# Kernel tuning notes

Hardware: AMD Instinct MI355X
Metric: run time of the kernel (lower is better)

Reference implementation:

```python
import jax, jax.numpy as jnp
import numpy as np

B, NQ, NC, D, H = 4, 4096, 4096, 1024, 16
HD = D // H
LN_EPS = 1e-5


def _layernorm(x, g, b):
    mu = jnp.mean(x, axis=-1, keepdims=True)
    var = jnp.var(x, axis=-1, keepdims=True)
    return (x - mu) * jax.lax.rsqrt(var + LN_EPS) * g + b


def _kernel(x):
    # elu(x) + 1  (strictly positive feature map)
    return jax.nn.elu(x) + 1.0


def setup_inputs() -> dict:
    key = jax.random.key(0)
    ks = jax.random.split(key, 12)
    s = 1.0 / np.sqrt(D)
    return {
        "query": jax.random.normal(ks[0], (B, NQ, D), jnp.float32),
        "context": jax.random.normal(ks[1], (B, NC, D), jnp.float32),
        "q_w": jax.random.uniform(ks[2], (D, D), jnp.float32, -s, s),
        "q_b": jnp.zeros((D,), jnp.float32),
        "k_w": jax.random.uniform(ks[3], (D, D), jnp.float32, -s, s),
        "k_b": jnp.zeros((D,), jnp.float32),
        "v_w": jax.random.uniform(ks[4], (D, D), jnp.float32, -s, s),
        "v_b": jnp.zeros((D,), jnp.float32),
        "o_w": jax.random.uniform(ks[5], (D, D), jnp.float32, -s, s),
        "o_b": jnp.zeros((D,), jnp.float32),
        "lnq_g": jnp.ones((D,), jnp.float32),
        "lnq_b": jnp.zeros((D,), jnp.float32),
        "lnkv_g": jnp.ones((D,), jnp.float32),
        "lnkv_b": jnp.zeros((D,), jnp.float32),
    }


def reference(query, context, q_w, q_b, k_w, k_b, v_w, v_b, o_w, o_b,
              lnq_g, lnq_b, lnkv_g, lnkv_b):
    residual = query
    q = _layernorm(query, lnq_g, lnq_b)
    c = _layernorm(context, lnkv_g, lnkv_b)

    # torch Linear: y = x @ W.T + b ; reshape to (B, H, N, Hd)
    Q = (q @ q_w.T + q_b).reshape(B, NQ, H, HD).transpose(0, 2, 1, 3)
    K = (c @ k_w.T + k_b).reshape(B, NC, H, HD).transpose(0, 2, 1, 3)
    V = (c @ v_w.T + v_b).reshape(B, NC, H, HD).transpose(0, 2, 1, 3)

    Q = _kernel(Q)
    K = _kernel(K)

    # KV: (B, H, Hd, Hd) outer-product accumulation over context length
    KV = jnp.einsum("bhnd,bhne->bhde", K, V)
    K_sum = K.sum(axis=2)                              # (B, H, Hd)
    Z = jnp.einsum("bhqd,bhd->bhq", Q, K_sum)          # (B, H, Nq)
    Z = jnp.maximum(Z, 1e-6)

    out = jnp.einsum("bhqd,bhde->bhqe", Q, KV) / Z[..., None]
    out = out.transpose(0, 2, 1, 3).reshape(B, NQ, D)
    return residual + (out @ o_w.T + o_b)
```

## Files before the change

kernel.cpp:

```cpp
#include <hip/hip_runtime.h>

#define DEV __device__ __forceinline__

typedef __attribute__((ext_vector_type(8))) short short8;
typedef __attribute__((ext_vector_type(4))) short short4v;
typedef __attribute__((ext_vector_type(4))) float f32x4;

DEV float bf2f(unsigned short u) { return __uint_as_float(((unsigned int)u) << 16); }
DEV unsigned short f2bf(float f) {
    unsigned int u = __float_as_uint(f);
    u += 0x7FFFu + ((u >> 16) & 1u);
    return (unsigned short)(u >> 16);
}

DEV void gload_lds16(const void* g, void* l) {
    __builtin_amdgcn_global_load_lds(
        (__attribute__((address_space(1))) unsigned int*)(g),
        (__attribute__((address_space(3))) unsigned int*)(l),
        16, 0, 0);
}

#define NROW 16384
#define DDIM 1024

__global__ __launch_bounds__(256) void ln_kernel(
    const float* __restrict__ query, const float* __restrict__ context,
    const float* __restrict__ lnq_g, const float* __restrict__ lnq_b,
    const float* __restrict__ lnk_g, const float* __restrict__ lnk_b,
    unsigned short* __restrict__ qln, unsigned short* __restrict__ cln)
{
    const int row = blockIdx.x;
    const bool isq = row < NROW;
    const int r = isq ? row : row - NROW;
    const float* src = (isq ? query : context) + (size_t)r * DDIM;
    const float* g   = isq ? lnq_g : lnk_g;
    const float* bb  = isq ? lnq_b : lnk_b;
    unsigned short* dst = (isq ? qln : cln) + (size_t)r * DDIM;

    const int tid = threadIdx.x;
    f32x4 x = *(const f32x4*)(src + tid * 4);
    float s  = x[0] + x[1] + x[2] + x[3];
    float sq = x[0]*x[0] + x[1]*x[1] + x[2]*x[2] + x[3]*x[3];
#pragma unroll
    for (int off = 32; off; off >>= 1) {
        s  += __shfl_xor(s, off);
        sq += __shfl_xor(sq, off);
    }
    __shared__ float red[8];
    const int lane = tid & 63, w = tid >> 6;
    if (lane == 0) { red[w] = s; red[4 + w] = sq; }
    __syncthreads();
    s  = red[0] + red[1] + red[2] + red[3];
    sq = red[4] + red[5] + red[6] + red[7];
    const float mu  = s * (1.0f / DDIM);
    const float var = sq * (1.0f / DDIM) - mu * mu;
    const float rstd = rsqrtf(var + 1e-5f);

    f32x4 gv = *(const f32x4*)(g + tid * 4);
    f32x4 bv = *(const f32x4*)(bb + tid * 4);
    short4v o;
#pragma unroll
    for (int j = 0; j < 4; ++j)
        o[j] = (short)f2bf((x[j] - mu) * rstd * gv[j] + bv[j]);
    *(short4v*)(dst + tid * 4) = o;
}

__global__ __launch_bounds__(256) void conv_w(
    const float* __restrict__ a, const float* __restrict__ b,
    const float* __restrict__ c, const float* __restrict__ d,
    unsigned short* __restrict__ out)
{
    const int i = blockIdx.x * 256 + threadIdx.x;
    const int mat = i >> 18;
    const int idx = (i & 262143) * 4;
    const float* src = mat == 0 ? a : mat == 1 ? b : mat == 2 ? c : d;
    f32x4 v = *(const f32x4*)(src + idx);
    short4v o;
#pragma unroll
    for (int j = 0; j < 4; ++j) o[j] = (short)f2bf(v[j]);
    *(short4v*)(out + (size_t)mat * 1048576 + idx) = o;
}

template <int MODE>
__global__ __launch_bounds__(512, 2) void gemm_bt(
    const unsigned short* __restrict__ A, const unsigned short* __restrict__ Bm,
    void* __restrict__ Cout, const float* __restrict__ bias,
    const float* __restrict__ resid, int ldc)
{
    __shared__ __attribute__((aligned(16))) unsigned short smem[65536];
    unsigned short* sAb = smem;
    unsigned short* sBb = smem + 32768;

    const int bid = blockIdx.x;
    const int l = (bid & 7) * 32 + (bid >> 3);
    int m0, n0;
    if (MODE == 0 || MODE == 3) { m0 = (l >> 2) * 256; n0 = (l & 3) * 256; }
    else                        { m0 = (l & 3) * 256;  n0 = (l >> 2) * 256; }

    const int tid = threadIdx.x;
    const int lane = tid & 63, w = tid >> 6;
    const int wr = w >> 2, wc = w & 3;
    const int lr = lane & 15, lg = lane >> 4;

    const int srow = tid >> 3;
    const int cswz = (tid & 7) ^ (srow & 7);
    const unsigned short* gA0 = A  + (size_t)(m0 + srow) * 1024 + cswz * 8;
    const unsigned short* gB0 = Bm + (size_t)(n0 + srow) * 1024 + cswz * 8;

    const int sw0 = ((0 + lg) ^ (lr & 7)) * 8;
    const int sw1 = ((4 + lg) ^ (lr & 7)) * 8;

    f32x4 acc[8][4];
#pragma unroll
    for (int i = 0; i < 8; ++i)
#pragma unroll
        for (int j = 0; j < 4; ++j)
#pragma unroll
            for (int e = 0; e < 4; ++e) acc[i][j][e] = 0.0f;

#define STG(GP, SP, T)                                                        \
    {                                                                         \
        const unsigned short* g = (GP) + (T) * 64;                            \
        unsigned short* d = (SP) + ((T) & 1) * 16384 + tid * 8;               \
        _Pragma("unroll")                                                     \
        for (int L = 0; L < 4; ++L)                                           \
            gload_lds16(g + (size_t)L * 65536, d + L * 4096);                 \
    }

    STG(gB0, sBb, 0); STG(gA0, sAb, 0); STG(gB0, sBb, 1); STG(gA0, sAb, 1);

    for (int t = 0; t < 16; ++t) {
        const unsigned short* bA = sAb + (t & 1) * 16384;
        const unsigned short* bB = sBb + (t & 1) * 16384;
        short8 afl[4][2], afh[4][2], bvl[2][2], bvh[2][2];

        if (t == 15) asm volatile("s_waitcnt vmcnt(0)" ::: "memory");
        else         asm volatile("s_waitcnt vmcnt(8)" ::: "memory");
        __builtin_amdgcn_s_barrier();
#pragma unroll
        for (int mt = 0; mt < 4; ++mt) {
            const int ra = (wr * 128 + mt * 16 + lr) * 64;
            afl[mt][0] = *(const short8*)&bA[ra + sw0];
            afl[mt][1] = *(const short8*)&bA[ra + sw1];
        }
#pragma unroll
        for (int nt = 0; nt < 2; ++nt) {
            const int rb = (wc * 64 + nt * 16 + lr) * 64;
            bvl[nt][0] = *(const short8*)&bB[rb + sw0];
            bvl[nt][1] = *(const short8*)&bB[rb + sw1];
        }
        __builtin_amdgcn_s_setprio(1);
#pragma unroll
        for (int kk = 0; kk < 2; ++kk)
#pragma unroll
            for (int mt = 0; mt < 4; ++mt)
#pragma unroll
                for (int nt = 0; nt < 2; ++nt)
                    acc[mt][nt] = __builtin_amdgcn_mfma_f32_16x16x32_bf16(
                        afl[mt][kk], bvl[nt][kk], acc[mt][nt], 0, 0, 0);
        __builtin_amdgcn_s_setprio(0);
        asm volatile("s_waitcnt lgkmcnt(0)" ::: "memory");
        __builtin_amdgcn_s_barrier();

#pragma unroll
        for (int nt = 0; nt < 2; ++nt) {
            const int rb = (wc * 64 + (nt + 2) * 16 + lr) * 64;
            bvh[nt][0] = *(const short8*)&bB[rb + sw0];
            bvh[nt][1] = *(const short8*)&bB[rb + sw1];
        }
        __builtin_amdgcn_s_setprio(1);
#pragma unroll
        for (int kk = 0; kk < 2; ++kk)
#pragma unroll
            for (int mt = 0; mt < 4; ++mt)
#pragma unroll
                for (int nt = 0; nt < 2; ++nt)
                    acc[mt][nt + 2] = __builtin_amdgcn_mfma_f32_16x16x32_bf16(
                        afl[mt][kk], bvh[nt][kk], acc[mt][nt + 2], 0, 0, 0);
        __builtin_amdgcn_s_setprio(0);
        asm volatile("s_waitcnt lgkmcnt(0)" ::: "memory");
        __builtin_amdgcn_s_barrier();

#pragma unroll
        for (int mt = 0; mt < 4; ++mt) {
            const int ra = (wr * 128 + (mt + 4) * 16 + lr) * 64;
            afh[mt][0] = *(const short8*)&bA[ra + sw0];
            afh[mt][1] = *(const short8*)&bA[ra + sw1];
        }
        if (t + 2 < 16) STG(gB0, sBb, t + 2);
        __builtin_amdgcn_s_setprio(1);
#pragma unroll
        for (int kk = 0; kk < 2; ++kk)
#pragma unroll
            for (int mt = 0; mt < 4; ++mt)
#pragma unroll
                for (int nt = 0; nt < 2; ++nt)
                    acc[mt + 4][nt + 2] = __builtin_amdgcn_mfma_f32_16x16x32_bf16(
                        afh[mt][kk], bvh[nt][kk], acc[mt + 4][nt + 2], 0, 0, 0);
        __builtin_amdgcn_s_setprio(0);
        asm volatile("s_waitcnt lgkmcnt(0)" ::: "memory");
        __builtin_amdgcn_s_barrier();

        if (t + 2 < 16) STG(gA0, sAb, t + 2);
        __builtin_amdgcn_s_setprio(1);
#pragma unroll
        for (int kk = 0; kk < 2; ++kk)
#pragma unroll
            for (int mt = 0; mt < 4; ++mt)
#pragma unroll
                for (int nt = 0; nt < 2; ++nt)
                    acc[mt + 4][nt] = __builtin_amdgcn_mfma_f32_16x16x32_bf16(
                        afh[mt][kk], bvl[nt][kk], acc[mt + 4][nt], 0, 0, 0);
        __builtin_amdgcn_s_setprio(0);
    }
#undef STG

#pragma unroll
    for (int mt = 0; mt < 8; ++mt) {
#pragma unroll
        for (int nt = 0; nt < 4; ++nt) {
            const int col = n0 + wc * 64 + nt * 16 + lr;
#pragma unroll
            for (int i = 0; i < 4; ++i) {
                const int row = m0 + wr * 128 + mt * 16 + lg * 4 + i;
                float v = acc[mt][nt][i];
                if (MODE == 0) { v += bias[col]; v = v > 0.0f ? v + 1.0f : __expf(v); }
                if (MODE == 1) { v += bias[row]; v = v > 0.0f ? v + 1.0f : __expf(v); }
                if (MODE == 2) { v += bias[row]; }
                if (MODE == 3) { v += bias[col] + resid[(size_t)row * 1024 + col]; }
                if (MODE == 3)
                    ((float*)Cout)[(size_t)row * 1024 + col] = v;
                else
                    ((unsigned short*)Cout)[(size_t)row * (size_t)ldc + col] = f2bf(v);
            }
        }
    }
}

__global__ __launch_bounds__(256) void kv_kernel(
    const unsigned short* __restrict__ VT, const unsigned short* __restrict__ KT,
    float* __restrict__ KVTp)
{
    const int bh = blockIdx.x, sp = blockIdx.y;
    const int b = bh >> 4, h = bh & 15;
    const int tid = threadIdx.x, lane = tid & 63, w = tid >> 6;
    const int lr = lane & 15, lg = lane >> 4;

    f32x4 acc[4][4];
#pragma unroll
    for (int i = 0; i < 4; ++i)
#pragma unroll
        for (int j = 0; j < 4; ++j)
#pragma unroll
            for (int e = 0; e < 4; ++e) acc[i][j][e] = 0.0f;

    const size_t colbase = (size_t)b * 4096 + sp * 1024 + w * 256 + lg * 8;
    const unsigned short* va = VT + (size_t)(h * 64 + lr) * NROW + colbase;
    const unsigned short* ka = KT + (size_t)(h * 64 + lr) * NROW + colbase;

    for (int ks = 0; ks < 8; ++ks) {
        short8 af[4], bfv[4];
#pragma unroll
        for (int mt = 0; mt < 4; ++mt)
            af[mt] = *(const short8*)(va + (size_t)mt * 16 * NROW + ks * 32);
#pragma unroll
        for (int nt = 0; nt < 4; ++nt)
            bfv[nt] = *(const short8*)(ka + (size_t)nt * 16 * NROW + ks * 32);
#pragma unroll
        for (int mt = 0; mt < 4; ++mt)
#pragma unroll
            for (int nt = 0; nt < 4; ++nt)
                acc[mt][nt] = __builtin_amdgcn_mfma_f32_16x16x32_bf16(
                    af[mt], bfv[nt], acc[mt][nt], 0, 0, 0);
    }

    __shared__ float red4[4][4096];
#pragma unroll
    for (int mt = 0; mt < 4; ++mt)
#pragma unroll
        for (int nt = 0; nt < 4; ++nt)
#pragma unroll
            for (int i = 0; i < 4; ++i)
                red4[w][(mt * 16 + lg * 4 + i) * 64 + nt * 16 + lr] = acc[mt][nt][i];
    __syncthreads();
    float* out = KVTp + ((size_t)sp * 64 + bh) * 4096;
    for (int i = tid; i < 4096; i += 256)
        out[i] = red4[0][i] + red4[1][i] + red4[2][i] + red4[3][i];
}

__global__ __launch_bounds__(256) void ksum_kernel(
    const unsigned short* __restrict__ KT, float* __restrict__ Ksum)
{
    const int bh = blockIdx.x, quad = blockIdx.y;
    const int b = bh >> 4, h = bh & 15;
    const int tid = threadIdx.x, lane = tid & 63, w = tid >> 6;
    const int dbase = quad * 16 + w * 4;
#pragma unroll
    for (int dd = 0; dd < 4; ++dd) {
        const int d = dbase + dd;
        const unsigned short* p = KT + (size_t)(h * 64 + d) * NROW + b * 4096 + lane * 8;
        float s = 0.0f;
#pragma unroll
        for (int it = 0; it < 8; ++it) {
            short8 v = *(const short8*)(p + it * 512);
#pragma unroll
            for (int j = 0; j < 8; ++j) s += bf2f((unsigned short)v[j]);
        }
#pragma unroll
        for (int off = 32; off; off >>= 1) s += __shfl_xor(s, off);
        if (lane == 0) Ksum[bh * 64 + d] = s;
    }
}

__global__ __launch_bounds__(256) void z_kernel(
    const unsigned short* __restrict__ Q, const float* __restrict__ Ksum,
    float* __restrict__ invZ)
{
    const int gid = blockIdx.x * 256 + threadIdx.x;
    const int n = gid >> 4, h = gid & 15;
    const int b = n >> 12;
    const unsigned short* q = Q + (size_t)n * DDIM + h * 64;
    const float* ks = Ksum + ((b << 4) + h) * 64;
    float z = 0.0f;
#pragma unroll
    for (int it = 0; it < 8; ++it) {
        short8 v = *(const short8*)(q + it * 8);
#pragma unroll
        for (int j = 0; j < 8; ++j) z += bf2f((unsigned short)v[j]) * ks[it * 8 + j];
    }
    invZ[gid] = 1.0f / fmaxf(z, 1e-6f);
}

__global__ __launch_bounds__(256) void a2_kernel(
    const unsigned short* __restrict__ Q, const float* __restrict__ KVTp,
    const float* __restrict__ invZ, unsigned short* __restrict__ A2)
{
    const int m0 = blockIdx.x * 128, h = blockIdx.y;
    const int b = m0 >> 12, bh = (b << 4) + h;
    const int tid = threadIdx.x, lane = tid & 63, w = tid >> 6;
    const int wr = w >> 1, wc = w & 1;
    const int lr = lane & 15, lg = lane >> 4;

    f32x4 acc[4][2];
#pragma unroll
    for (int i = 0; i < 4; ++i)
#pragma unroll
        for (int j = 0; j < 2; ++j)
#pragma unroll
            for (int e = 0; e < 4; ++e) acc[i][j][e] = 0.0f;

    const unsigned short* qa = Q + (size_t)(m0 + wr * 64 + lr) * DDIM + h * 64 + lg * 8;
    const float* kvb = KVTp + (size_t)bh * 4096 + (wc * 32 + lr) * 64 + lg * 8;

#pragma unroll
    for (int ks = 0; ks < 2; ++ks) {
        short8 af[4];
#pragma unroll
        for (int mt = 0; mt < 4; ++mt)
            af[mt] = *(const short8*)(qa + (size_t)mt * 16 * DDIM + ks * 32);
        short8 bfv[2];
#pragma unroll
        for (int nt = 0; nt < 2; ++nt) {
            const float* p = kvb + nt * 16 * 64 + ks * 32;
            short8 t;
#pragma unroll
            for (int j = 0; j < 8; ++j) {
                float v = p[j] + p[j + 262144] + p[j + 2 * 262144] + p[j + 3 * 262144];
                t[j] = (short)f2bf(v);
            }
            bfv[nt] = t;
        }
#pragma unroll
        for (int mt = 0; mt < 4; ++mt)
#pragma unroll
            for (int nt = 0; nt < 2; ++nt)
                acc[mt][nt] = __builtin_amdgcn_mfma_f32_16x16x32_bf16(
                    af[mt], bfv[nt], acc[mt][nt], 0, 0, 0);
    }

#pragma unroll
    for (int mt = 0; mt < 4; ++mt)
#pragma unroll
        for (int nt = 0; nt < 2; ++nt)
#pragma unroll
            for (int i = 0; i < 4; ++i) {
                const int row = m0 + wr * 64 + mt * 16 + lg * 4 + i;
                const int col = h * 64 + wc * 32 + nt * 16 + lr;
                const float v = acc[mt][nt][i] * invZ[row * 16 + h];
                A2[(size_t)row * DDIM + col] = f2bf(v);
            }
}

extern "C" void kernel_launch(void* const* d_in, const int* in_sizes, int n_in,
                              void* d_out, int out_size, void* d_ws, size_t ws_size,
                              hipStream_t stream)
{
    const float* query   = (const float*)d_in[0];
    const float* context = (const float*)d_in[1];
    const float* q_w = (const float*)d_in[2];
    const float* q_b = (const float*)d_in[3];
    const float* k_w = (const float*)d_in[4];
    const float* k_b = (const float*)d_in[5];
    const float* v_w = (const float*)d_in[6];
    const float* v_b = (const float*)d_in[7];
    const float* o_w = (const float*)d_in[8];
    const float* o_b = (const float*)d_in[9];
    const float* lnq_g = (const float*)d_in[10];
    const float* lnq_b = (const float*)d_in[11];
    const float* lnk_g = (const float*)d_in[12];
    const float* lnk_b = (const float*)d_in[13];

    char* ws = (char*)d_ws;
    unsigned short* WQ  = (unsigned short*)(ws);
    unsigned short* WK  = (unsigned short*)(ws + (2u << 20));
    unsigned short* WV  = (unsigned short*)(ws + (4u << 20));
    unsigned short* WO  = (unsigned short*)(ws + (6u << 20));
    unsigned short* QLN = (unsigned short*)(ws + (8u << 20));
    unsigned short* CLN = (unsigned short*)(ws + (40u << 20));
    unsigned short* Qm  = (unsigned short*)(ws + (72u << 20));
    unsigned short* KT  = (unsigned short*)(ws + (104u << 20));
    unsigned short* VT  = (unsigned short*)(ws + (136u << 20));
    float* KVTp = (float*)(ws + (168u << 20));
    float* Ksum = (float*)(ws + (172u << 20));
    float* invZ = (float*)(ws + (173u << 20));
    unsigned short* A2 = QLN;

    conv_w<<<4096, 256, 0, stream>>>(q_w, k_w, v_w, o_w, WQ);
    ln_kernel<<<2 * NROW, 256, 0, stream>>>(query, context, lnq_g, lnq_b,
                                            lnk_g, lnk_b, QLN, CLN);
    gemm_bt<0><<<256, 512, 0, stream>>>(QLN, WQ, Qm, q_b, nullptr, 1024);
    gemm_bt<1><<<256, 512, 0, stream>>>(WK, CLN, KT, k_b, nullptr, NROW);
    gemm_bt<2><<<256, 512, 0, stream>>>(WV, CLN, VT, v_b, nullptr, NROW);
    kv_kernel<<<dim3(64, 4), 256, 0, stream>>>(VT, KT, KVTp);
    ksum_kernel<<<dim3(64, 4), 256, 0, stream>>>(KT, Ksum);
    z_kernel<<<1024, 256, 0, stream>>>(Qm, Ksum, invZ);
    a2_kernel<<<dim3(128, 16), 256, 0, stream>>>(Qm, KVTp, invZ, A2);
    gemm_bt<3><<<256, 512, 0, stream>>>(A2, WO, d_out, o_b, query, 1024);
}
```

Before: 277.5 us.

## Reschedule GEMM main loop to prefetch next-tile B fragments across iterations

Restructures the 4-phase MFMA main loop so the low B fragments for the next K-tile are loaded from LDS during the current iteration and carried over in registers. It uses partial lgkmcnt waits instead of full drains, and reorders the quadrant computations and the global-to-LDS staging points. The aim is to overlap LDS reads with MFMA work and drop one barrier-plus-full-wait per iteration. In exchange it raises register pressure, and the waitcnt and barrier ordering is delicate: a vmcnt(0) each iteration could expose global load latency.

Result: no change. 273.6 us (-1.4%).

```diff
diff --git a/kernel.cpp b/kernel.cpp
--- a/kernel.cpp
+++ b/kernel.cpp
@@ -128,15 +128,23 @@
     }
 
     STG(gB0, sBb, 0); STG(gA0, sAb, 0); STG(gB0, sBb, 1); STG(gA0, sAb, 1);
+    asm volatile("s_waitcnt vmcnt(8)" ::: "memory");
+    __builtin_amdgcn_s_barrier();
+
+    short8 bvl[2][2];
+#pragma unroll
+    for (int nt = 0; nt < 2; ++nt) {
+        const int rb = (wc * 64 + nt * 16 + lr) * 64;
+        bvl[nt][0] = *(const short8*)&sBb[rb + sw0];
+        bvl[nt][1] = *(const short8*)&sBb[rb + sw1];
+    }
 
     for (int t = 0; t < 16; ++t) {
         const unsigned short* bA = sAb + (t & 1) * 16384;
         const unsigned short* bB = sBb + (t & 1) * 16384;
-        short8 afl[4][2], afh[4][2], bvl[2][2], bvh[2][2];
-
-        if (t == 15) asm volatile("s_waitcnt vmcnt(0)" ::: "memory");
-        else         asm volatile("s_waitcnt vmcnt(8)" ::: "memory");
-        __builtin_amdgcn_s_barrier();
+        const unsigned short* bBn = sBb + ((t + 1) & 1) * 16384;
+        short8 afl[4][2], afh[4][2], bvh[2][2], bvln[2][2];
+
 #pragma unroll
         for (int mt = 0; mt < 4; ++mt) {
             const int ra = (wr * 128 + mt * 16 + lr) * 64;
@@ -144,11 +152,12 @@
             afl[mt][1] = *(const short8*)&bA[ra + sw1];
         }
 #pragma unroll
-        for (int nt = 0; nt < 2; ++nt) {
-            const int rb = (wc * 64 + nt * 16 + lr) * 64;
-            bvl[nt][0] = *(const short8*)&bB[rb + sw0];
-            bvl[nt][1] = *(const short8*)&bB[rb + sw1];
-        }
+        for (int mt = 0; mt < 4; ++mt) {
+            const int ra = (wr * 128 + (mt + 4) * 16 + lr) * 64;
+            afh[mt][0] = *(const short8*)&bA[ra + sw0];
+            afh[mt][1] = *(const short8*)&bA[ra + sw1];
+        }
+        asm volatile("s_waitcnt lgkmcnt(8)" ::: "memory");
         __builtin_amdgcn_s_setprio(1);
 #pragma unroll
         for (int kk = 0; kk < 2; ++kk)
@@ -159,7 +168,6 @@
                     acc[mt][nt] = __builtin_amdgcn_mfma_f32_16x16x32_bf16(
                         afl[mt][kk], bvl[nt][kk], acc[mt][nt], 0, 0, 0);
         __builtin_amdgcn_s_setprio(0);
-        asm volatile("s_waitcnt lgkmcnt(0)" ::: "memory");
         __builtin_amdgcn_s_barrier();
 
 #pragma unroll
@@ -168,6 +176,44 @@
             bvh[nt][0] = *(const short8*)&bB[rb + sw0];
             bvh[nt][1] = *(const short8*)&bB[rb + sw1];
         }
+        asm volatile("s_waitcnt lgkmcnt(4)" ::: "memory");
+        __builtin_amdgcn_s_setprio(1);
+#pragma unroll
+        for (int kk = 0; kk < 2; ++kk)
+#pragma unroll
+            for (int mt = 0; mt < 4; ++mt)
+#pragma unroll
+                for (int nt = 0; nt < 2; ++nt)
+                    acc[mt + 4][nt] = __builtin_amdgcn_mfma_f32_16x16x32_bf16(
+                        afh[mt][kk], bvl[nt][kk], acc[mt + 4][nt], 0, 0, 0);
+        __builtin_amdgcn_s_setprio(0);
+        asm volatile("s_waitcnt vmcnt(0)" ::: "memory");
+        __builtin_amdgcn_s_barrier();
+
+        if (t < 15) {
+#pragma unroll
+            for (int nt = 0; nt < 2; ++nt) {
+                const int rb = (wc * 64 + nt * 16 + lr) * 64;
+                bvln[nt][0] = *(const short8*)&bBn[rb + sw0];
+                bvln[nt][1] = *(const short8*)&bBn[rb + sw1];
+            }
+        }
+        if (t + 2 < 16) STG(gA0, sAb, t + 2);
+        if (t < 15) asm volatile("s_waitcnt lgkmcnt(4)" ::: "memory");
+        else        asm volatile("s_waitcnt lgkmcnt(0)" ::: "memory");
+        __builtin_amdgcn_s_setprio(1);
+#pragma unroll
+        for (int kk = 0; kk < 2; ++kk)
+#pragma unroll
+            for (int mt = 0; mt < 4; ++mt)
+#pragma unroll
+                for (int nt = 0; nt < 2; ++nt)
+                    acc[mt + 4][nt + 2] = __builtin_amdgcn_mfma_f32_16x16x32_bf16(
+                        afh[mt][kk], bvh[nt][kk], acc[mt + 4][nt + 2], 0, 0, 0);
+        __builtin_amdgcn_s_setprio(0);
+        __builtin_amdgcn_s_barrier();
+
+        if (t + 2 < 16) STG(gB0, sBb, t + 2);
         __builtin_amdgcn_s_setprio(1);
 #pragma unroll
         for (int kk = 0; kk < 2; ++kk)
@@ -178,40 +224,14 @@
                     acc[mt][nt + 2] = __builtin_amdgcn_mfma_f32_16x16x32_bf16(
                         afl[mt][kk], bvh[nt][kk], acc[mt][nt + 2], 0, 0, 0);
         __builtin_amdgcn_s_setprio(0);
-        asm volatile("s_waitcnt lgkmcnt(0)" ::: "memory");
-        __builtin_amdgcn_s_barrier();
-
-#pragma unroll
-        for (int mt = 0; mt < 4; ++mt) {
-            const int ra = (wr * 128 + (mt + 4) * 16 + lr) * 64;
-            afh[mt][0] = *(const short8*)&bA[ra + sw0];
-            afh[mt][1] = *(const short8*)&bA[ra + sw1];
-        }
-        if (t + 2 < 16) STG(gB0, sBb, t + 2);
-        __builtin_amdgcn_s_setprio(1);
-#pragma unroll
-        for (int kk = 0; kk < 2; ++kk)
-#pragma unroll
-            for (int mt = 0; mt < 4; ++mt)
-#pragma unroll
-                for (int nt = 0; nt < 2; ++nt)
-                    acc[mt + 4][nt + 2] = __builtin_amdgcn_mfma_f32_16x16x32_bf16(
-                        afh[mt][kk], bvh[nt][kk], acc[mt + 4][nt + 2], 0, 0, 0);
-        __builtin_amdgcn_s_setprio(0);
-        asm volatile("s_waitcnt lgkmcnt(0)" ::: "memory");
-        __builtin_amdgcn_s_barrier();
-
-        if (t + 2 < 16) STG(gA0, sAb, t + 2);
-        __builtin_amdgcn_s_setprio(1);
-#pragma unroll
-        for (int kk = 0; kk < 2; ++kk)
-#pragma unroll
-            for (int mt = 0; mt < 4; ++mt)
-#pragma unroll
-                for (int nt = 0; nt < 2; ++nt)
-                    acc[mt + 4][nt] = __builtin_amdgcn_mfma_f32_16x16x32_bf16(
-                        afh[mt][kk], bvl[nt][kk], acc[mt + 4][nt], 0, 0, 0);
-        __builtin_amdgcn_s_setprio(0);
+
+        if (t < 15) {
+#pragma unroll
+            for (int nt = 0; nt < 2; ++nt) {
+                bvl[nt][0] = bvln[nt][0];
+                bvl[nt][1] = bvln[nt][1];
+            }
+        }
     }
 #undef STG
 
```
